# Kernel optimization log

Hardware: AMD Instinct MI355X
Metric: run time of the kernel (lower is better)

The kernel has to match this reference:

```python
import jax, jax.numpy as jnp
import numpy as np

D = 1024   # dim_embedding
H = 16     # n_head
HD = D // H


def setup_inputs() -> dict:
    key = jax.random.key(0)
    ks = jax.random.split(key, 5)
    B, T = 2, 2048
    x = jax.random.normal(ks[0], (B, T, D), dtype=jnp.float32)
    e = jax.random.normal(ks[1], (B, T, D), dtype=jnp.float32)
    s = 0.02
    W_en = jax.random.normal(ks[2], (D, 2 * D), dtype=jnp.float32) * s   # c_attn_en (k,v from encoder)
    W_q = jax.random.normal(ks[3], (D, D), dtype=jnp.float32) * s        # c_attn (q from decoder)
    W_o = jax.random.normal(ks[4], (D, D), dtype=jnp.float32) * s        # c_proj
    return {"x": x, "e": e, "W_en": W_en, "W_q": W_q, "W_o": W_o}


def reference(x, e, W_en, W_q, W_o):
    B, T, C = e.shape
    kv = e @ W_en                       # [B,T,2C]
    k, v = jnp.split(kv, 2, axis=-1)    # [B,T,C] each
    q = x @ W_q                         # [B,T,C]
    # reshape to heads: [B,H,T,hd]
    q = q.reshape(B, T, H, HD).transpose(0, 2, 1, 3)
    k = k.reshape(B, T, H, HD).transpose(0, 2, 1, 3)
    v = v.reshape(B, T, H, HD).transpose(0, 2, 1, 3)
    att = jnp.einsum("bhqd,bhkd->bhqk", q, k) * (1.0 / jnp.sqrt(jnp.float32(HD)))
    att = jax.nn.softmax(att, axis=-1)  # dropout=0 (eval)
    y = jnp.einsum("bhqk,bhkd->bhqd", att, v)
    y = y.transpose(0, 2, 1, 3).reshape(B, T, C)
    return y @ W_o
```

## Files before the change

### kernel.cpp

```cpp
#include <hip/hip_runtime.h>

typedef unsigned short u16;
typedef unsigned int u32;
typedef __bf16 bf16x8 __attribute__((ext_vector_type(8)));
typedef float f32x4 __attribute__((ext_vector_type(4)));
typedef float f32x16 __attribute__((ext_vector_type(16)));

#define D_EMB 1024
#define T_SEQ 2048
#define NH 16
#define HD 64

#define GLB(p) ((const __attribute__((address_space(1))) unsigned int*)(p))
#define LDSP(p) ((__attribute__((address_space(3))) unsigned int*)(p))

__device__ __forceinline__ u16 f2bf(float f) {
  union { float f; unsigned u; } c; c.f = f;
  unsigned u = c.u;
  unsigned r = (u + 0x7FFFu + ((u >> 16) & 1u)) >> 16;
  return (u16)r;
}
__device__ __forceinline__ u32 fbits(float f) {
  union { float f; unsigned u; } c; c.f = f; return c.u;
}

__global__ __launch_bounds__(256) void prep_kernel(
    const float* __restrict__ x, const float* __restrict__ e,
    const float* __restrict__ W_q, const float* __restrict__ W_en, const float* __restrict__ W_o,
    u16* __restrict__ xb, u16* __restrict__ eb,
    u16* __restrict__ Wqt, u16* __restrict__ Went, u16* __restrict__ Wot) {
  __shared__ float tile[32][33];
  const int bid = blockIdx.x, tid = threadIdx.x;
  if (bid < 8192) {
    const float* in = (bid < 4096) ? x : e;
    u16* out = (bid < 4096) ? xb : eb;
    int i = (bid & 4095) * 256 + tid;
    float4 v = reinterpret_cast<const float4*>(in)[i];
    ushort4 o;
    o.x = f2bf(v.x); o.y = f2bf(v.y); o.z = f2bf(v.z); o.w = f2bf(v.w);
    reinterpret_cast<ushort4*>(out)[i] = o;
    return;
  }
  const float* in; u16* out; int K, N, bx, by;
  int rem = bid - 8192;
  if (rem < 1024)      { in = W_q;  out = Wqt;  K = 1024; N = 1024; bx = rem & 31;          by = rem >> 5; }
  else if (rem < 3072) { int r2 = rem - 1024; in = W_en; out = Went; K = 1024; N = 2048; bx = r2 & 63; by = r2 >> 6; }
  else                 { int r3 = rem - 3072; in = W_o;  out = Wot;  K = 1024; N = 1024; bx = r3 & 31; by = r3 >> 5; }
  int tx = tid & 31, ty = tid >> 5;
  int n0 = bx * 32, k0 = by * 32;
#pragma unroll
  for (int s = 0; s < 4; s++)
    tile[ty + 8 * s][tx] = in[(size_t)(k0 + ty + 8 * s) * N + n0 + tx];
  __syncthreads();
#pragma unroll
  for (int s = 0; s < 4; s++)
    out[(size_t)(n0 + ty + 8 * s) * K + k0 + tx] = f2bf(tile[tx][ty + 8 * s]);
}

__global__ __launch_bounds__(256) void proj_kernel(
    const u16* __restrict__ xb, const u16* __restrict__ eb,
    const u16* __restrict__ Wqt, const u16* __restrict__ Went,
    u16* __restrict__ qw, u16* __restrict__ kw, u16* __restrict__ vTw) {
  __shared__ u16 Al[128 * 64];
  __shared__ u16 Bl[128 * 64];
  const int tid = threadIdx.x;
  const int nb = blockIdx.x, mb = blockIdx.y;
  const int wave = tid >> 6, lane = tid & 63;
  const int ln15 = lane & 15, quad = lane >> 4;
  const int wm = wave & 1, wn = wave >> 1;

  const u16* A = (nb < 8) ? xb : eb;
  const u16* Wt = (nb < 8) ? (Wqt + (size_t)nb * 128 * D_EMB)
                           : (Went + ((size_t)nb * 128 - D_EMB) * D_EMB);

  const int grow = wave * 8 + (lane >> 3);
  const int g = (lane & 7) ^ ((lane >> 3) & 7);
  const u16* gA = A + (size_t)(mb * 128 + grow) * D_EMB + g * 8;
  const u16* gB = Wt + (size_t)grow * D_EMB + g * 8;
  char* lA = (char*)Al + wave * 1024;
  char* lB = (char*)Bl + wave * 1024;

  f32x4 acc[4][4] = {};

  for (int kb = 0; kb < D_EMB; kb += 64) {
#pragma unroll
    for (int it = 0; it < 4; it++) {
      __builtin_amdgcn_global_load_lds(GLB(gA + (size_t)it * 32 * D_EMB + kb), LDSP(lA + it * 4096), 16, 0, 0);
      __builtin_amdgcn_global_load_lds(GLB(gB + (size_t)it * 32 * D_EMB + kb), LDSP(lB + it * 4096), 16, 0, 0);
    }
    __syncthreads();
#pragma unroll
    for (int ks = 0; ks < 2; ks++) {
      bf16x8 af[4], bfr[4];
#pragma unroll
      for (int mt = 0; mt < 4; mt++) {
        int r = wm * 64 + mt * 16 + ln15;
        af[mt] = *reinterpret_cast<const bf16x8*>(&Al[r * 64 + (((ks * 4 + quad) ^ (r & 7)) * 8)]);
      }
#pragma unroll
      for (int nt = 0; nt < 4; nt++) {
        int r = wn * 64 + nt * 16 + ln15;
        bfr[nt] = *reinterpret_cast<const bf16x8*>(&Bl[r * 64 + (((ks * 4 + quad) ^ (r & 7)) * 8)]);
      }
#pragma unroll
      for (int mt = 0; mt < 4; mt++)
#pragma unroll
        for (int nt = 0; nt < 4; nt++)
          acc[mt][nt] = __builtin_amdgcn_mfma_f32_16x16x32_bf16(af[mt], bfr[nt], acc[mt][nt], 0, 0, 0);
    }
    __syncthreads();
  }

  const float QSCL = 0.125f * 1.44269504f;
#pragma unroll
  for (int mt = 0; mt < 4; mt++) {
#pragma unroll
    for (int nt = 0; nt < 4; nt++) {
#pragma unroll
      for (int i = 0; i < 4; i++) {
        int rr = mb * 128 + wm * 64 + mt * 16 + quad * 4 + i;
        int c  = nb * 128 + wn * 64 + nt * 16 + ln15;
        float v = acc[mt][nt][i];
        int b = rr >> 11, t = rr & 2047;
        if (c < D_EMB) {
          int h = c >> 6, d = c & 63;
          qw[(((size_t)(b * NH + h)) * T_SEQ + t) * HD + d] = f2bf(v * QSCL);
        } else if (c < 2 * D_EMB) {
          int cc = c - D_EMB; int h = cc >> 6, d = cc & 63;
          kw[(((size_t)(b * NH + h)) * T_SEQ + t) * HD + d] = f2bf(v);
        } else {
          int cc = c - 2 * D_EMB; int h = cc >> 6, d = cc & 63;
          vTw[(((size_t)(b * NH + h)) * HD + d) * T_SEQ + t] = f2bf(v);
        }
      }
    }
  }
}

__global__ __launch_bounds__(256) void attn_kernel(
    const u16* __restrict__ q, const u16* __restrict__ k,
    const u16* __restrict__ vT, u16* __restrict__ y) {
  __shared__ u16 Kl[2][64][64];
  __shared__ u16 Vl[2][64][64];
  __shared__ u16 Pl[4][32][64];

  const int bh = blockIdx.y;
  const int qt = blockIdx.x;
  const int tid = threadIdx.x;
  const int wave = tid >> 6, lane = tid & 63;
  const int q32 = lane & 31, hi = lane >> 5;
  const int b = bh >> 4, h = bh & 15;

  const int qrow = qt * 128 + wave * 32 + q32;
  const u16* qbase = q + ((size_t)bh * T_SEQ + qrow) * HD;
  bf16x8 qf[4];
#pragma unroll
  for (int s = 0; s < 4; s++)
    qf[s] = *reinterpret_cast<const bf16x8*>(qbase + s * 16 + hi * 8);

  f32x16 o2[2] = {};
  float lp = 0.f;

  const int srow = (lane >> 3) & 7;
  const int gch  = (lane & 7) ^ srow;
  const u16* kg0 = k  + ((size_t)bh * T_SEQ + wave * 16 + srow) * HD + gch * 8;
  const u16* vg0 = vT + ((size_t)bh * HD + wave * 16 + srow) * T_SEQ + gch * 8;

  auto issue_dma = [&](int t, int buf) {
    char* klb = (char*)&Kl[buf][0][0] + wave * 2048;
    char* vlb = (char*)&Vl[buf][0][0] + wave * 2048;
    const u16* kp = kg0 + (size_t)t * 64 * HD;
    const u16* vp = vg0 + t * 64;
    __builtin_amdgcn_global_load_lds(GLB(kp),           LDSP(klb),        16, 0, 0);
    __builtin_amdgcn_global_load_lds(GLB(kp + 8 * HD),  LDSP(klb + 1024), 16, 0, 0);
    __builtin_amdgcn_global_load_lds(GLB(vp),           LDSP(vlb),        16, 0, 0);
    __builtin_amdgcn_global_load_lds(GLB(vp + 8 * T_SEQ), LDSP(vlb + 1024), 16, 0, 0);
  };

  issue_dma(0, 0);

  for (int t = 0; t < 32; t++) {
    const int buf = t & 1;
    __syncthreads();
    if (t < 31) issue_dma(t + 1, buf ^ 1);

    f32x16 s2[2] = {};
#pragma unroll
    for (int s = 0; s < 4; s++)
#pragma unroll
      for (int kt2 = 0; kt2 < 2; kt2++) {
        int r = kt2 * 32 + q32;
        bf16x8 kf = *reinterpret_cast<const bf16x8*>(
            &Kl[buf][r][(((s * 2 + hi) ^ (r & 7)) * 8)]);
        s2[kt2] = __builtin_amdgcn_mfma_f32_32x32x16_bf16(kf, qf[s], s2[kt2], 0, 0, 0);
      }

#pragma unroll
    for (int kt2 = 0; kt2 < 2; kt2++)
#pragma unroll
      for (int g = 0; g < 4; g++) {
        float p0 = __builtin_amdgcn_exp2f(s2[kt2][4 * g + 0]);
        float p1 = __builtin_amdgcn_exp2f(s2[kt2][4 * g + 1]);
        float p2 = __builtin_amdgcn_exp2f(s2[kt2][4 * g + 2]);
        float p3 = __builtin_amdgcn_exp2f(s2[kt2][4 * g + 3]);
        lp += (p0 + p1) + (p2 + p3);
        u32 dw0 = __builtin_amdgcn_perm(fbits(p1), fbits(p0), 0x07060302u);
        u32 dw1 = __builtin_amdgcn_perm(fbits(p3), fbits(p2), 0x07060302u);
        int phys = (kt2 * 4 + g) ^ (q32 & 7);
        *reinterpret_cast<uint2*>(&Pl[wave][q32][phys * 8 + 4 * hi]) = make_uint2(dw0, dw1);
      }
    asm volatile("s_waitcnt lgkmcnt(0)" ::: "memory");

#pragma unroll
    for (int s = 0; s < 4; s++) {
      bf16x8 pf = *reinterpret_cast<const bf16x8*>(
          &Pl[wave][q32][(((s * 2 + hi) ^ (q32 & 7)) * 8)]);
#pragma unroll
      for (int dt = 0; dt < 2; dt++) {
        int r = dt * 32 + q32;
        bf16x8 vf = *reinterpret_cast<const bf16x8*>(
            &Vl[buf][r][(((s * 2 + hi) ^ (r & 7)) * 8)]);
        o2[dt] = __builtin_amdgcn_mfma_f32_32x32x16_bf16(vf, pf, o2[dt], 0, 0, 0);
      }
    }
  }

  lp += __shfl_xor(lp, 32, 64);
  const float inv = 1.0f / lp;

  const size_t ybase = ((size_t)b * T_SEQ + qrow) * D_EMB + h * 64;
#pragma unroll
  for (int dt = 0; dt < 2; dt++)
#pragma unroll
    for (int g = 0; g < 4; g++) {
      u16 b0 = f2bf(o2[dt][4 * g + 0] * inv), b1 = f2bf(o2[dt][4 * g + 1] * inv);
      u16 b2 = f2bf(o2[dt][4 * g + 2] * inv), b3 = f2bf(o2[dt][4 * g + 3] * inv);
      u32 dw0 = (u32)b0 | ((u32)b1 << 16);
      u32 dw1 = (u32)b2 | ((u32)b3 << 16);
      *reinterpret_cast<uint2*>(&y[ybase + dt * 32 + 8 * g + 4 * hi]) = make_uint2(dw0, dw1);
    }
}

__global__ __launch_bounds__(256) void oproj_kernel(
    const u16* __restrict__ yw, const u16* __restrict__ Wot, float* __restrict__ out) {
  __shared__ u16 Al[128 * 64];
  __shared__ u16 Bl[128 * 64];
  const int tid = threadIdx.x;
  const int nb = blockIdx.x, mb = blockIdx.y;
  const int wave = tid >> 6, lane = tid & 63;
  const int ln15 = lane & 15, quad = lane >> 4;
  const int wm = wave & 1, wn = wave >> 1;

  const u16* Wt = Wot + (size_t)nb * 128 * D_EMB;
  const int grow = wave * 8 + (lane >> 3);
  const int g = (lane & 7) ^ ((lane >> 3) & 7);
  const u16* gA = yw + (size_t)(mb * 128 + grow) * D_EMB + g * 8;
  const u16* gB = Wt + (size_t)grow * D_EMB + g * 8;
  char* lA = (char*)Al + wave * 1024;
  char* lB = (char*)Bl + wave * 1024;

  f32x4 acc[4][4] = {};

  for (int kb = 0; kb < D_EMB; kb += 64) {
#pragma unroll
    for (int it = 0; it < 4; it++) {
      __builtin_amdgcn_global_load_lds(GLB(gA + (size_t)it * 32 * D_EMB + kb), LDSP(lA + it * 4096), 16, 0, 0);
      __builtin_amdgcn_global_load_lds(GLB(gB + (size_t)it * 32 * D_EMB + kb), LDSP(lB + it * 4096), 16, 0, 0);
    }
    __syncthreads();
#pragma unroll
    for (int ks = 0; ks < 2; ks++) {
      bf16x8 af[4], bfr[4];
#pragma unroll
      for (int mt = 0; mt < 4; mt++) {
        int r = wm * 64 + mt * 16 + ln15;
        af[mt] = *reinterpret_cast<const bf16x8*>(&Al[r * 64 + (((ks * 4 + quad) ^ (r & 7)) * 8)]);
      }
#pragma unroll
      for (int nt = 0; nt < 4; nt++) {
        int r = wn * 64 + nt * 16 + ln15;
        bfr[nt] = *reinterpret_cast<const bf16x8*>(&Bl[r * 64 + (((ks * 4 + quad) ^ (r & 7)) * 8)]);
      }
#pragma unroll
      for (int mt = 0; mt < 4; mt++)
#pragma unroll
        for (int nt = 0; nt < 4; nt++)
          acc[mt][nt] = __builtin_amdgcn_mfma_f32_16x16x32_bf16(af[mt], bfr[nt], acc[mt][nt], 0, 0, 0);
    }
    __syncthreads();
  }

#pragma unroll
  for (int mt = 0; mt < 4; mt++)
#pragma unroll
    for (int nt = 0; nt < 4; nt++)
#pragma unroll
      for (int i = 0; i < 4; i++) {
        int rr = mb * 128 + wm * 64 + mt * 16 + quad * 4 + i;
        int c  = nb * 128 + wn * 64 + nt * 16 + ln15;
        out[(size_t)rr * D_EMB + c] = acc[mt][nt][i];
      }
}

extern "C" void kernel_launch(void* const* d_in, const int* in_sizes, int n_in,
                              void* d_out, int out_size, void* d_ws, size_t ws_size,
                              hipStream_t stream) {
  const float* x    = (const float*)d_in[0];
  const float* e    = (const float*)d_in[1];
  const float* W_en = (const float*)d_in[2];
  const float* W_q  = (const float*)d_in[3];
  const float* W_o  = (const float*)d_in[4];
  float* out = (float*)d_out;

  char* w = (char*)d_ws;
  u16* xb   = (u16*)(w);
  u16* eb   = (u16*)(w + (8u  << 20));
  u16* Wqt  = (u16*)(w + (16u << 20));
  u16* Went = (u16*)(w + (18u << 20));
  u16* Wot  = (u16*)(w + (22u << 20));
  u16* qw   = (u16*)(w + (24u << 20));
  u16* kw   = (u16*)(w + (32u << 20));
  u16* vT   = (u16*)(w + (40u << 20));
  u16* yw   = (u16*)(w + (48u << 20));

  prep_kernel<<<12288, 256, 0, stream>>>(x, e, W_q, W_en, W_o, xb, eb, Wqt, Went, Wot);
  proj_kernel<<<dim3(24, 32), 256, 0, stream>>>(xb, eb, Wqt, Went, qw, kw, vT);
  attn_kernel<<<dim3(T_SEQ / 128, 32), 256, 0, stream>>>(qw, kw, vT, yw);
  oproj_kernel<<<dim3(8, 32), 256, 0, stream>>>(yw, Wot, out);
}
```

Baseline: 225.3 us.

## Double-buffer LDS in projection GEMMs and halve oproj M-tile for more blocks

Both GEMM kernels now stage tiles into two LDS buffers and prefetch the next K-slice while computing the current one, removing the trailing barrier per iteration. The output projection also drops its M tile from 128 to 64 rows and doubles the grid to 512 blocks, giving better occupancy across the many CUs. The cost is twice the LDS footprint per block, and a smaller oproj tile means less data reuse per block.

```diff
diff --git a/kernel.cpp b/kernel.cpp
--- a/kernel.cpp
+++ b/kernel.cpp
@@ -43,7 +43,7 @@
   }
   const float* in; u16* out; int K, N, bx, by;
   int rem = bid - 8192;
-  if (rem < 1024)      { in = W_q;  out = Wqt;  K = 1024; N = 1024; bx = rem & 31;          by = rem >> 5; }
+  if (rem < 1024)      { in = W_q;  out = Wqt;  K = 1024; N = 1024; bx = rem & 31; by = rem >> 5; }
   else if (rem < 3072) { int r2 = rem - 1024; in = W_en; out = Went; K = 1024; N = 2048; bx = r2 & 63; by = r2 >> 6; }
   else                 { int r3 = rem - 3072; in = W_o;  out = Wot;  K = 1024; N = 1024; bx = r3 & 31; by = r3 >> 5; }
   int tx = tid & 31, ty = tid >> 5;
@@ -61,8 +61,8 @@
     const u16* __restrict__ xb, const u16* __restrict__ eb,
     const u16* __restrict__ Wqt, const u16* __restrict__ Went,
     u16* __restrict__ qw, u16* __restrict__ kw, u16* __restrict__ vTw) {
-  __shared__ u16 Al[128 * 64];
-  __shared__ u16 Bl[128 * 64];
+  __shared__ u16 Al[2][128 * 64];
+  __shared__ u16 Bl[2][128 * 64];
   const int tid = threadIdx.x;
   const int nb = blockIdx.x, mb = blockIdx.y;
   const int wave = tid >> 6, lane = tid & 63;
@@ -73,34 +73,40 @@
   const u16* Wt = (nb < 8) ? (Wqt + (size_t)nb * 128 * D_EMB)
                            : (Went + ((size_t)nb * 128 - D_EMB) * D_EMB);
 
+  const int g = (lane & 7) ^ ((lane >> 3) & 7);
   const int grow = wave * 8 + (lane >> 3);
-  const int g = (lane & 7) ^ ((lane >> 3) & 7);
   const u16* gA = A + (size_t)(mb * 128 + grow) * D_EMB + g * 8;
   const u16* gB = Wt + (size_t)grow * D_EMB + g * 8;
-  char* lA = (char*)Al + wave * 1024;
-  char* lB = (char*)Bl + wave * 1024;
-
-  f32x4 acc[4][4] = {};
-
-  for (int kb = 0; kb < D_EMB; kb += 64) {
+
+  auto stage = [&](int kb, int buf) {
+    char* lA = (char*)&Al[buf][0] + wave * 1024;
+    char* lB = (char*)&Bl[buf][0] + wave * 1024;
 #pragma unroll
     for (int it = 0; it < 4; it++) {
       __builtin_amdgcn_global_load_lds(GLB(gA + (size_t)it * 32 * D_EMB + kb), LDSP(lA + it * 4096), 16, 0, 0);
       __builtin_amdgcn_global_load_lds(GLB(gB + (size_t)it * 32 * D_EMB + kb), LDSP(lB + it * 4096), 16, 0, 0);
     }
+  };
+
+  f32x4 acc[4][4] = {};
+  stage(0, 0);
+
+  for (int t = 0; t < 16; t++) {
+    const int buf = t & 1;
     __syncthreads();
+    if (t < 15) stage((t + 1) * 64, buf ^ 1);
 #pragma unroll
     for (int ks = 0; ks < 2; ks++) {
       bf16x8 af[4], bfr[4];
 #pragma unroll
       for (int mt = 0; mt < 4; mt++) {
         int r = wm * 64 + mt * 16 + ln15;
-        af[mt] = *reinterpret_cast<const bf16x8*>(&Al[r * 64 + (((ks * 4 + quad) ^ (r & 7)) * 8)]);
+        af[mt] = *reinterpret_cast<const bf16x8*>(&Al[buf][r * 64 + (((ks * 4 + quad) ^ (r & 7)) * 8)]);
       }
 #pragma unroll
       for (int nt = 0; nt < 4; nt++) {
         int r = wn * 64 + nt * 16 + ln15;
-        bfr[nt] = *reinterpret_cast<const bf16x8*>(&Bl[r * 64 + (((ks * 4 + quad) ^ (r & 7)) * 8)]);
+        bfr[nt] = *reinterpret_cast<const bf16x8*>(&Bl[buf][r * 64 + (((ks * 4 + quad) ^ (r & 7)) * 8)]);
       }
 #pragma unroll
       for (int mt = 0; mt < 4; mt++)
@@ -108,7 +114,6 @@
         for (int nt = 0; nt < 4; nt++)
           acc[mt][nt] = __builtin_amdgcn_mfma_f32_16x16x32_bf16(af[mt], bfr[nt], acc[mt][nt], 0, 0, 0);
     }
-    __syncthreads();
   }
 
   const float QSCL = 0.125f * 1.44269504f;
@@ -171,9 +176,9 @@
     char* vlb = (char*)&Vl[buf][0][0] + wave * 2048;
     const u16* kp = kg0 + (size_t)t * 64 * HD;
     const u16* vp = vg0 + t * 64;
-    __builtin_amdgcn_global_load_lds(GLB(kp),           LDSP(klb),        16, 0, 0);
-    __builtin_amdgcn_global_load_lds(GLB(kp + 8 * HD),  LDSP(klb + 1024), 16, 0, 0);
-    __builtin_amdgcn_global_load_lds(GLB(vp),           LDSP(vlb),        16, 0, 0);
+    __builtin_amdgcn_global_load_lds(GLB(kp),             LDSP(klb),        16, 0, 0);
+    __builtin_amdgcn_global_load_lds(GLB(kp + 8 * HD),    LDSP(klb + 1024), 16, 0, 0);
+    __builtin_amdgcn_global_load_lds(GLB(vp),             LDSP(vlb),        16, 0, 0);
     __builtin_amdgcn_global_load_lds(GLB(vp + 8 * T_SEQ), LDSP(vlb + 1024), 16, 0, 0);
   };
 
@@ -243,60 +248,65 @@
 
 __global__ __launch_bounds__(256) void oproj_kernel(
     const u16* __restrict__ yw, const u16* __restrict__ Wot, float* __restrict__ out) {
-  __shared__ u16 Al[128 * 64];
-  __shared__ u16 Bl[128 * 64];
+  __shared__ u16 Al[2][64 * 64];
+  __shared__ u16 Bl[2][128 * 64];
   const int tid = threadIdx.x;
   const int nb = blockIdx.x, mb = blockIdx.y;
   const int wave = tid >> 6, lane = tid & 63;
   const int ln15 = lane & 15, quad = lane >> 4;
   const int wm = wave & 1, wn = wave >> 1;
 
-  const u16* Wt = Wot + (size_t)nb * 128 * D_EMB;
-  const int grow = wave * 8 + (lane >> 3);
-  const int g = (lane & 7) ^ ((lane >> 3) & 7);
-  const u16* gA = yw + (size_t)(mb * 128 + grow) * D_EMB + g * 8;
-  const u16* gB = Wt + (size_t)grow * D_EMB + g * 8;
-  char* lA = (char*)Al + wave * 1024;
-  char* lB = (char*)Bl + wave * 1024;
-
-  f32x4 acc[4][4] = {};
-
-  for (int kb = 0; kb < D_EMB; kb += 64) {
-#pragma unroll
-    for (int it = 0; it < 4; it++) {
-      __builtin_amdgcn_global_load_lds(GLB(gA + (size_t)it * 32 * D_EMB + kb), LDSP(lA + it * 4096), 16, 0, 0);
-      __builtin_amdgcn_global_load_lds(GLB(gB + (size_t)it * 32 * D_EMB + kb), LDSP(lB + it * 4096), 16, 0, 0);
-    }
+  const int srow = lane >> 3;
+  const int g = (lane & 7) ^ (srow & 7);
+  const u16* gA = yw  + (size_t)(mb * 64 + wave * 16 + srow) * D_EMB + g * 8;
+  const u16* gB = Wot + (size_t)(nb * 128 + wave * 32 + srow) * D_EMB + g * 8;
+
+  auto stage = [&](int kb, int buf) {
+    char* lA = (char*)&Al[buf][0] + wave * 2048;
+    char* lB = (char*)&Bl[buf][0] + wave * 4096;
+#pragma unroll
+    for (int it = 0; it < 2; it++)
+      __builtin_amdgcn_global_load_lds(GLB(gA + (size_t)it * 8 * D_EMB + kb), LDSP(lA + it * 1024), 16, 0, 0);
+#pragma unroll
+    for (int it = 0; it < 4; it++)
+      __builtin_amdgcn_global_load_lds(GLB(gB + (size_t)it * 8 * D_EMB + kb), LDSP(lB + it * 1024), 16, 0, 0);
+  };
+
+  f32x4 acc[2][4] = {};
+  stage(0, 0);
+
+  for (int t = 0; t < 16; t++) {
+    const int buf = t & 1;
     __syncthreads();
+    if (t < 15) stage((t + 1) * 64, buf ^ 1);
 #pragma unroll
     for (int ks = 0; ks < 2; ks++) {
-      bf16x8 af[4], bfr[4];
-#pragma unroll
-      for (int mt = 0; mt < 4; mt++) {
-        int r = wm * 64 + mt * 16 + ln15;
-        af[mt] = *reinterpret_cast<const bf16x8*>(&Al[r * 64 + (((ks * 4 + quad) ^ (r & 7)) * 8)]);
+      bf16x8 af[2], bfr[4];
+#pragma unroll
+      for (int mt = 0; mt < 2; mt++) {
+        int r = wm * 32 + mt * 16 + ln15;
+        af[mt] = *reinterpret_cast<const bf16x8*>(&Al[buf][r * 64 + (((ks * 4 + quad) ^ (r & 7)) * 8)]);
       }
 #pragma unroll
       for (int nt = 0; nt < 4; nt++) {
         int r = wn * 64 + nt * 16 + ln15;
-        bfr[nt] = *reinterpret_cast<const bf16x8*>(&Bl[r * 64 + (((ks * 4 + quad) ^ (r & 7)) * 8)]);
-      }
-#pragma unroll
-      for (int mt = 0; mt < 4; mt++)
+        bfr[nt] = *reinterpret_cast<const bf16x8*>(&Bl[buf][r * 64 + (((ks * 4 + quad) ^ (r & 7)) * 8)]);
+      }
+#pragma unroll
+      for (int mt = 0; mt < 2; mt++)
 #pragma unroll
         for (int nt = 0; nt < 4; nt++)
           acc[mt][nt] = __builtin_amdgcn_mfma_f32_16x16x32_bf16(af[mt], bfr[nt], acc[mt][nt], 0, 0, 0);
     }
-    __syncthreads();
-  }
-
-#pragma unroll
-  for (int mt = 0; mt < 4; mt++)
+  }
+
+#pragma unroll
+  for (int mt = 0; mt < 2; mt++)
 #pragma unroll
     for (int nt = 0; nt < 4; nt++)
 #pragma unroll
       for (int i = 0; i < 4; i++) {
-        int rr = mb * 128 + wm * 64 + mt * 16 + quad * 4 + i;
+        int rr = mb * 64 + wm * 32 + mt * 16 + quad * 4 + i;
         int c  = nb * 128 + wn * 64 + nt * 16 + ln15;
         out[(size_t)rr * D_EMB + c] = acc[mt][nt][i];
       }
@@ -326,5 +336,5 @@
   prep_kernel<<<12288, 256, 0, stream>>>(x, e, W_q, W_en, W_o, xb, eb, Wqt, Went, Wot);
   proj_kernel<<<dim3(24, 32), 256, 0, stream>>>(xb, eb, Wqt, Went, qw, kw, vT);
   attn_kernel<<<dim3(T_SEQ / 128, 32), 256, 0, stream>>>(qw, kw, vT, yw);
-  oproj_kernel<<<dim3(8, 32), 256, 0, stream>>>(yw, Wot, out);
-}
+  oproj_kernel<<<dim3(8, 64), 256, 0, stream>>>(yw, Wot, out);
+}
```

Measured after the change: 230.8 us. +2.5%, slower.
